# Kernel optimization log

Hardware: AMD Instinct MI355X
Metric: run time of the kernel (lower is better)

Reference implementation:

```python
import jax, jax.numpy as jnp
import numpy as np

N_NODES = 100000
N_EDGES = 3200000
IN_F = 128


def gcn_conv(x, edge_index, edge_weight, W, b):
    """PyG GCNConv: add self-loops (weight 1), symmetric normalization,
    scatter-add aggregation from src -> dst, then bias."""
    n = x.shape[0]
    src, dst = edge_index[0], edge_index[1]
    h = x @ W  # [N, out]
    # degree with self-loop weight 1
    deg = jax.ops.segment_sum(edge_weight, dst, num_segments=n) + 1.0
    dinv = jax.lax.rsqrt(deg)
    norm = dinv[src] * edge_weight * dinv[dst]  # [E]
    msgs = norm[:, None] * h[src]  # [E, out]
    out = jax.ops.segment_sum(msgs, dst, num_segments=n)
    # self-loop contribution: norm = dinv*1*dinv = 1/deg
    out = out + h / deg[:, None]
    return out + b


def setup_inputs() -> dict:
    key = jax.random.key(0)
    ks = jax.random.split(key, 12)
    x = jax.random.normal(ks[0], (N_NODES, IN_F), dtype=jnp.float32)
    edge_index = jax.random.randint(ks[1], (2, N_EDGES), 0, N_NODES)
    edge_weights = jax.random.uniform(ks[2], (N_EDGES,), dtype=jnp.float32)
    def glorot(k, shape):
        lim = np.sqrt(6.0 / (shape[0] + shape[1]))
        return jax.random.uniform(k, shape, jnp.float32, -lim, lim)
    return {
        "x": x,
        "edge_index": edge_index,
        "edge_weights": edge_weights,
        "W1": glorot(ks[3], (IN_F, 32)),
        "b1": jnp.zeros((32,), jnp.float32),
        "W2": glorot(ks[4], (32, 16)),
        "b2": jnp.zeros((16,), jnp.float32),
        "fc1_w": glorot(ks[5], (16, 1)),
        "fc1_b": jnp.zeros((1,), jnp.float32),
        "fc2_w": glorot(ks[6], (33, 1)),
        "fc2_b": jnp.zeros((1,), jnp.float32),
    }


def reference(x, edge_index, edge_weights, W1, b1, W2, b2, fc1_w, fc1_b, fc2_w, fc2_b):
    x1 = gcn_conv(x, edge_index, edge_weights, W1, b1)
    h = jax.nn.relu(x1)  # dropout is identity in eval mode
    x2 = gcn_conv(h, edge_index, edge_weights, W2, b2)
    x1f = x2 @ fc1_w + fc1_b        # [N, 1]
    c = jax.nn.sigmoid(x1f)
    cat = jnp.concatenate([h, c], axis=1)  # [N, 33]
    r = cat @ fc2_w + fc2_b         # [N, 1]
    return (r, x1f)
```

## Files before the change

kernel.cpp:

```cpp
#include <hip/hip_runtime.h>
#include <math.h>


#define TPB 256
#define PA_CHUNK 4096
#define KMAXB 512
#define NPW 8

__global__ __launch_bounds__(512) void countA_kernel(const int* __restrict__ dst,
                                                     int* __restrict__ gtot,
                                                     int E, int K) {
    __shared__ int lhist[KMAXB];
    const int tid = threadIdx.x;
    const int e0  = blockIdx.x * PA_CHUNK;
    if (tid < KMAXB) lhist[tid] = 0;
    __syncthreads();
#pragma unroll
    for (int i = 0; i < 8; ++i) {
        int e = e0 + tid + i * 512;
        if (e < E) atomicAdd(&lhist[dst[e] >> 8], 1);
    }
    __syncthreads();
    if (tid < K && lhist[tid] > 0) atomicAdd(&gtot[tid], lhist[tid]);
}

__global__ __launch_bounds__(64) void kscan_kernel(const int* __restrict__ gtot,
                                                   int* __restrict__ gstart,
                                                   int* __restrict__ gcursor,
                                                   int K, int E) {
    int tid = threadIdx.x;
    int b0 = tid * 8, v[8], s = 0;
#pragma unroll
    for (int t = 0; t < 8; ++t) {
        v[t] = s;
        int idx = b0 + t;
        s += (idx < K) ? gtot[idx] : 0;
    }
    int incl = s;
#pragma unroll
    for (int d = 1; d < 64; d <<= 1) {
        int t2 = __shfl_up(incl, d);
        if (tid >= d) incl += t2;
    }
    int excl = incl - s;
#pragma unroll
    for (int t = 0; t < 8; ++t) {
        int idx = b0 + t;
        if (idx < K) { gstart[idx] = excl + v[t]; gcursor[idx] = excl + v[t]; }
    }
    if (tid == 63) gstart[K] = E;
}

__global__ __launch_bounds__(512) void placeA_kernel(const int* __restrict__ src,
                                                     const int* __restrict__ dst,
                                                     const float* __restrict__ ew,
                                                     uint2* __restrict__ tmp,
                                                     int* __restrict__ gcursor,
                                                     int E, int K) {
    __shared__ int lhist[KMAXB], lbase[KMAXB], lcur[KMAXB], gbaseS[KMAXB];
    __shared__ int ltot;
    __shared__ uint2 stage[PA_CHUNK];
    __shared__ int   saddr[PA_CHUNK];
    const int tid = threadIdx.x;
    const int e0  = blockIdx.x * PA_CHUNK;

    if (tid < KMAXB) { lhist[tid] = 0; lcur[tid] = 0; }
    __syncthreads();

    int   b[8];
    uint2 p[8];
#pragma unroll
    for (int i = 0; i < 8; ++i) {
        int e = e0 + tid + i * 512;
        b[i] = -1;
        if (e < E) {
            int d   = dst[e];
            int s   = src[e];
            float w = ew[e];
            b[i]   = d >> 8;
            p[i].x = __float_as_uint(w);
            p[i].y = ((unsigned)s << 8) | (unsigned)(d & 255);
            atomicAdd(&lhist[b[i]], 1);
        }
    }
    __syncthreads();

    if (tid < 64) {
        int b0 = tid * 8, v[8], s = 0;
#pragma unroll
        for (int t = 0; t < 8; ++t) { v[t] = s; s += lhist[b0 + t]; }
        int incl = s;
#pragma unroll
        for (int d = 1; d < 64; d <<= 1) {
            int t2 = __shfl_up(incl, d);
            if (tid >= d) incl += t2;
        }
        int excl = incl - s;
#pragma unroll
        for (int t = 0; t < 8; ++t) lbase[b0 + t] = excl + v[t];
        if (tid == 63) ltot = incl;
    }
    __syncthreads();

    if (tid < K && lhist[tid] > 0)
        gbaseS[tid] = atomicAdd(&gcursor[tid], lhist[tid]);
    __syncthreads();

#pragma unroll
    for (int i = 0; i < 8; ++i) {
        if (b[i] >= 0) {
            int r    = atomicAdd(&lcur[b[i]], 1);
            int sidx = lbase[b[i]] + r;
            stage[sidx] = p[i];
            saddr[sidx] = gbaseS[b[i]] + r;
        }
    }
    __syncthreads();

    int tot = ltot;
    for (int s = tid; s < tot; s += 512) tmp[saddr[s]] = stage[s];
}

__global__ __launch_bounds__(512) void partB_kernel(const uint2* __restrict__ tmp,
                                                    const int* __restrict__ gstart,
                                                    int2* __restrict__ epair,
                                                    int* __restrict__ off,
                                                    float* __restrict__ dinv,
                                                    int N) {
    __shared__ int   lhist[256], loff[256], lcur[256];
    __shared__ float ldeg[256];
    const int tid  = threadIdx.x;
    const int k    = blockIdx.x;
    const int seg0 = gstart[k], seg1 = gstart[k + 1];

    if (tid < 256) { lhist[tid] = 0; lcur[tid] = 0; ldeg[tid] = 0.f; }
    __syncthreads();

    for (int j = seg0 + tid; j < seg1; j += 512)
        atomicAdd(&lhist[tmp[j].y & 255u], 1);
    __syncthreads();

    if (tid < 64) {
        int b0 = tid * 4, v[4], s = 0;
#pragma unroll
        for (int t = 0; t < 4; ++t) { v[t] = s; s += lhist[b0 + t]; }
        int incl = s;
#pragma unroll
        for (int d = 1; d < 64; d <<= 1) {
            int t2 = __shfl_up(incl, d);
            if (tid >= d) incl += t2;
        }
        int excl = incl - s;
#pragma unroll
        for (int t = 0; t < 4; ++t) loff[b0 + t] = excl + v[t];
    }
    __syncthreads();

    if (tid < 256) {
        int d = (k << 8) + tid;
        if (d < N) off[d] = seg0 + loff[tid];
    }

    for (int j = seg0 + tid; j < seg1; j += 512) {
        uint2 q  = tmp[j];
        int dlow = q.y & 255u;
        int s    = (int)(q.y >> 8);
        float w  = __uint_as_float(q.x);
        int r    = atomicAdd(&lcur[dlow], 1);
        int2 pr; pr.x = s; pr.y = (int)q.x;
        epair[seg0 + loff[dlow] + r] = pr;
        atomicAdd(&ldeg[dlow], w);
    }
    __syncthreads();

    if (tid < 256) {
        int d = (k << 8) + tid;
        if (d < N) dinv[d] = 1.0f / sqrtf(ldeg[tid] + 1.0f);
    }
}

__global__ __launch_bounds__(TPB) void gemm1_kernel(const float* __restrict__ x,
                                                    const float* __restrict__ W,
                                                    const float* __restrict__ dinv,
                                                    float* __restrict__ h, int N) {
    __shared__ float Ws[128 * 32];
    __shared__ float xs[32 * 129];
    const int tid = threadIdx.x;
    const int nb  = blockIdx.x * 32;

    const float4* W4  = (const float4*)W;
    float4*       Ws4 = (float4*)Ws;
#pragma unroll
    for (int i = 0; i < 4; ++i) Ws4[tid + i * 256] = W4[tid + i * 256];

#pragma unroll
    for (int i = 0; i < 4; ++i) {
        int idx  = tid + i * 256;
        int node = idx >> 5;
        int col4 = idx & 31;
        if (nb + node < N) {
            float4 v = ((const float4*)(x + (size_t)nb * 128))[idx];
            float* p = &xs[node * 129 + col4 * 4];
            p[0] = v.x; p[1] = v.y; p[2] = v.z; p[3] = v.w;
        }
    }
    __syncthreads();

    const int nl = tid >> 3;
    const int og = (tid & 7) * 4;
    float a0 = 0.f, a1 = 0.f, a2 = 0.f, a3 = 0.f;
#pragma unroll 8
    for (int k = 0; k < 128; ++k) {
        float xv = xs[nl * 129 + k];
        const float* wp = &Ws[k * 32 + og];
        a0 = fmaf(xv, wp[0], a0);
        a1 = fmaf(xv, wp[1], a1);
        a2 = fmaf(xv, wp[2], a2);
        a3 = fmaf(xv, wp[3], a3);
    }
    int node = nb + nl;
    if (node < N) {
        float dv = dinv[node];
        float* out = &h[(size_t)node * 32 + og];
        out[0] = a0 * dv; out[1] = a1 * dv; out[2] = a2 * dv; out[3] = a3 * dv;
    }
}

__global__ __launch_bounds__(TPB) void gather32_fused_kernel(
    const int* __restrict__ off, const int2* __restrict__ epair,
    const float* __restrict__ g1, const float* __restrict__ dinv,
    const float* __restrict__ b1, const float* __restrict__ W2,
    const float* __restrict__ fc1_w, const float* __restrict__ fc2_w,
    float* __restrict__ z, float* __restrict__ rdot, int N, int E) {
    __shared__ float wls[560];
    const int tid = threadIdx.x;
    wls[tid]       = W2[tid];
    wls[tid + 256] = W2[tid + 256];
    if (tid < 32)      wls[512 + tid] = fc2_w[tid];
    else if (tid < 48) wls[512 + tid] = fc1_w[tid - 32];
    __syncthreads();

    const int lane = tid & 63;
    const int f    = lane & 31;
    const int half = lane >> 5;
    const float bv = b1[f];
    const int wbase = (lane < 16) ? lane : 512;
    const int wstrd = (lane < 16) ? 16 : 1;
    const float f1v = wls[544 + (lane & 15)];

    const int i0 = (blockIdx.x * (TPB / 64) + (tid >> 6)) * NPW;

    for (int t = 0; t < NPW; ++t) {
        int i = i0 + t;
        if (i >= N) return;
        const int s0 = off[i];
        const int s1 = (i + 1 < N) ? off[i + 1] : E;

        float acc = 0.f;
        int j = s0 + half;
        for (; j + 6 < s1; j += 8) {
            int2 pa = epair[j];
            int2 pb = epair[j + 2];
            int2 pc = epair[j + 4];
            int2 pd = epair[j + 6];
            acc = fmaf(__int_as_float(pa.y), g1[(size_t)pa.x * 32 + f], acc);
            acc = fmaf(__int_as_float(pb.y), g1[(size_t)pb.x * 32 + f], acc);
            acc = fmaf(__int_as_float(pc.y), g1[(size_t)pc.x * 32 + f], acc);
            acc = fmaf(__int_as_float(pd.y), g1[(size_t)pd.x * 32 + f], acc);
        }
        for (; j < s1; j += 2) {
            int2 p = epair[j];
            acc = fmaf(__int_as_float(p.y), g1[(size_t)p.x * 32 + f], acc);
        }
        acc += __shfl_xor(acc, 32);

        float dv = dinv[i];
        float v  = fmaxf(dv * (acc + g1[(size_t)i * 32 + f]) + bv, 0.f);

        float hs = 0.f;
#pragma unroll
        for (int k = 0; k < 32; ++k)
            hs = fmaf(__shfl(v, k), wls[wbase + k * wstrd], hs);

        float zp = hs * dv * f1v;
        zp += __shfl_xor(zp, 1);
        zp += __shfl_xor(zp, 2);
        zp += __shfl_xor(zp, 4);
        zp += __shfl_xor(zp, 8);

        if (lane == 0)       z[i]    = zp;
        else if (lane == 16) rdot[i] = hs;
    }
}

__global__ __launch_bounds__(TPB) void final_scalar_kernel(
    const int* __restrict__ off, const int2* __restrict__ epair,
    const float* __restrict__ z, const float* __restrict__ rdot,
    const float* __restrict__ dinv, const float* __restrict__ b2,
    const float* __restrict__ fc1_w, const float* __restrict__ fc1_b,
    const float* __restrict__ fc2_w, const float* __restrict__ fc2_b,
    float* __restrict__ out, int N, int E) {
    const int tid  = threadIdx.x;
    const int lane = tid & 63;

    float C = fc1_b[0];
#pragma unroll
    for (int f = 0; f < 16; ++f) C = fmaf(b2[f], fc1_w[f], C);
    const float f2w = fc2_w[32];
    const float f2b = fc2_b[0];

    const int i0 = (blockIdx.x * (TPB / 64) + (tid >> 6)) * NPW;

    for (int t = 0; t < NPW; ++t) {
        int i = i0 + t;
        if (i >= N) return;
        const int s0 = off[i];
        const int s1 = (i + 1 < N) ? off[i + 1] : E;

        float acc = 0.f;
        for (int j = s0 + lane; j < s1; j += 64) {
            int2 p = epair[j];
            acc = fmaf(__int_as_float(p.y), z[p.x], acc);
        }
        acc += __shfl_xor(acc, 1);
        acc += __shfl_xor(acc, 2);
        acc += __shfl_xor(acc, 4);
        acc += __shfl_xor(acc, 8);
        acc += __shfl_xor(acc, 16);
        acc += __shfl_xor(acc, 32);

        float x1f = dinv[i] * (acc + z[i]) + C;
        float c   = 1.0f / (1.0f + expf(-x1f));
        float r   = fmaf(c, f2w, f2b) + rdot[i];

        if (lane == 0) {
            out[i]     = r;
            out[N + i] = x1f;
        }
    }
}

extern "C" void kernel_launch(void* const* d_in, const int* in_sizes, int n_in,
                              void* d_out, int out_size, void* d_ws, size_t ws_size,
                              hipStream_t stream) {
    const float* x     = (const float*)d_in[0];
    const int*   ei    = (const int*)d_in[1];
    const float* ew    = (const float*)d_in[2];
    const float* W1    = (const float*)d_in[3];
    const float* b1    = (const float*)d_in[4];
    const float* W2    = (const float*)d_in[5];
    const float* b2    = (const float*)d_in[6];
    const float* fc1_w = (const float*)d_in[7];
    const float* fc1_b = (const float*)d_in[8];
    const float* fc2_w = (const float*)d_in[9];
    const float* fc2_b = (const float*)d_in[10];

    const int N = in_sizes[0] / 128;
    const int E = in_sizes[2];
    const int* src = ei;
    const int* dst = ei + E;
    const int K = (N + 255) >> 8;

    float* ws    = (float*)d_ws;
    float* dinv  = ws;
    float* big   = dinv + N;
    float* g1    = big;
    float* rdot  = big + (size_t)48 * N;
    float* z     = big + (size_t)49 * N;
    int*   off   = (int*)(big + (size_t)64 * N);
    int2*  epair = (int2*)(off + N);
    int*   gcursor = (int*)(epair + E);
    int*   gstart  = gcursor + K;
    uint2* tmp   = (uint2*)big;

    size_t need = ((size_t)66 * N + (size_t)2 * E + 2 * K + 2) * 4;
    if (ws_size < need || K > KMAXB || (size_t)E > (size_t)32 * N) return;

    hipMemsetAsync(gcursor, 0, (size_t)K * sizeof(int), stream);

    countA_kernel<<<(E + PA_CHUNK - 1) / PA_CHUNK, 512, 0, stream>>>(dst, gcursor, E, K);
    kscan_kernel<<<1, 64, 0, stream>>>(gcursor, gstart, gcursor, K, E);
    placeA_kernel<<<(E + PA_CHUNK - 1) / PA_CHUNK, 512, 0, stream>>>(
        src, dst, ew, tmp, gcursor, E, K);
    partB_kernel<<<K, 512, 0, stream>>>(tmp, gstart, epair, off, dinv, N);

    gemm1_kernel<<<(N + 31) / 32, TPB, 0, stream>>>(x, W1, dinv, g1, N);

    const int gblocks = (N + 4 * NPW - 1) / (4 * NPW);
    gather32_fused_kernel<<<gblocks, TPB, 0, stream>>>(
        off, epair, g1, dinv, b1, W2, fc1_w, fc2_w, z, rdot, N, E);
    final_scalar_kernel<<<gblocks, TPB, 0, stream>>>(
        off, epair, z, rdot, dinv, b2, fc1_w, fc1_b, fc2_w, fc2_b,
        (float*)d_out, N, E);
}
```

Measured before the change: 350.3 us.

## Fuse edge placement with first GEMM and sort buckets in-place via LDS

Shrinks destination buckets from 256 to 128 nodes so each bucket's edges fit in LDS during the second partition pass. That pass now sorts in place in the edge buffer instead of writing a separate pair array, and spills to scratch when a bucket overflows. The unscaled first-layer GEMM runs as extra blocks of the placement kernel, so the two overlap. The dinv scaling of g1 moves into the partition kernel as a read-modify-write. In exchange, the partition kernel does extra global traffic on g1, and the fused kernel uses larger shared memory, which may lower occupancy.

After: 359.6 us. 1.03x slower.

```diff
diff --git a/kernel.cpp b/kernel.cpp
--- a/kernel.cpp
+++ b/kernel.cpp
@@ -3,8 +3,12 @@
 
 
 #define TPB 256
-#define PA_CHUNK 4096
-#define KMAXB 512
+#define CNT_CHUNK 4096
+#define PLC_CHUNK 3584
+#define KMAXB 1024
+#define BSH 7
+#define BMSK 127
+#define PB_CAP 6912
 #define NPW 8
 
 __global__ __launch_bounds__(512) void countA_kernel(const int* __restrict__ dst,
@@ -12,26 +16,28 @@
                                                      int E, int K) {
     __shared__ int lhist[KMAXB];
     const int tid = threadIdx.x;
-    const int e0  = blockIdx.x * PA_CHUNK;
-    if (tid < KMAXB) lhist[tid] = 0;
+    const int e0  = blockIdx.x * CNT_CHUNK;
+    lhist[tid] = 0; lhist[tid + 512] = 0;
     __syncthreads();
 #pragma unroll
     for (int i = 0; i < 8; ++i) {
         int e = e0 + tid + i * 512;
-        if (e < E) atomicAdd(&lhist[dst[e] >> 8], 1);
+        if (e < E) atomicAdd(&lhist[dst[e] >> BSH], 1);
     }
     __syncthreads();
-    if (tid < K && lhist[tid] > 0) atomicAdd(&gtot[tid], lhist[tid]);
+    for (int b = tid; b < K; b += 512)
+        if (lhist[b] > 0) atomicAdd(&gtot[b], lhist[b]);
 }
 
 __global__ __launch_bounds__(64) void kscan_kernel(const int* __restrict__ gtot,
                                                    int* __restrict__ gstart,
                                                    int* __restrict__ gcursor,
+                                                   int* __restrict__ spill,
                                                    int K, int E) {
     int tid = threadIdx.x;
-    int b0 = tid * 8, v[8], s = 0;
-#pragma unroll
-    for (int t = 0; t < 8; ++t) {
+    int b0 = tid * 13, v[13], s = 0;
+#pragma unroll
+    for (int t = 0; t < 13; ++t) {
         v[t] = s;
         int idx = b0 + t;
         s += (idx < K) ? gtot[idx] : 0;
@@ -44,185 +50,237 @@
     }
     int excl = incl - s;
 #pragma unroll
-    for (int t = 0; t < 8; ++t) {
+    for (int t = 0; t < 13; ++t) {
         int idx = b0 + t;
         if (idx < K) { gstart[idx] = excl + v[t]; gcursor[idx] = excl + v[t]; }
     }
-    if (tid == 63) gstart[K] = E;
-}
-
-__global__ __launch_bounds__(512) void placeA_kernel(const int* __restrict__ src,
+    if (tid == 0) { gstart[K] = E; spill[0] = 0; }
+}
+
+__global__ __launch_bounds__(512) void fusedA_kernel(const int* __restrict__ src,
                                                      const int* __restrict__ dst,
                                                      const float* __restrict__ ew,
-                                                     uint2* __restrict__ tmp,
+                                                     uint2* __restrict__ ebuf,
                                                      int* __restrict__ gcursor,
-                                                     int E, int K) {
-    __shared__ int lhist[KMAXB], lbase[KMAXB], lcur[KMAXB], gbaseS[KMAXB];
-    __shared__ int ltot;
-    __shared__ uint2 stage[PA_CHUNK];
-    __shared__ int   saddr[PA_CHUNK];
+                                                     const float* __restrict__ x,
+                                                     const float* __restrict__ W,
+                                                     float* __restrict__ h,
+                                                     int E, int K, int N, int PB) {
+    __shared__ __align__(16) char smem[59392];
     const int tid = threadIdx.x;
-    const int e0  = blockIdx.x * PA_CHUNK;
-
-    if (tid < KMAXB) { lhist[tid] = 0; lcur[tid] = 0; }
-    __syncthreads();
-
-    int   b[8];
-    uint2 p[8];
-#pragma unroll
-    for (int i = 0; i < 8; ++i) {
-        int e = e0 + tid + i * 512;
-        b[i] = -1;
-        if (e < E) {
-            int d   = dst[e];
-            int s   = src[e];
-            float w = ew[e];
-            b[i]   = d >> 8;
-            p[i].x = __float_as_uint(w);
-            p[i].y = ((unsigned)s << 8) | (unsigned)(d & 255);
-            atomicAdd(&lhist[b[i]], 1);
-        }
-    }
-    __syncthreads();
-
-    if (tid < 64) {
-        int b0 = tid * 8, v[8], s = 0;
-#pragma unroll
-        for (int t = 0; t < 8; ++t) { v[t] = s; s += lhist[b0 + t]; }
-        int incl = s;
-#pragma unroll
-        for (int d = 1; d < 64; d <<= 1) {
-            int t2 = __shfl_up(incl, d);
-            if (tid >= d) incl += t2;
-        }
-        int excl = incl - s;
-#pragma unroll
-        for (int t = 0; t < 8; ++t) lbase[b0 + t] = excl + v[t];
-        if (tid == 63) ltot = incl;
-    }
-    __syncthreads();
-
-    if (tid < K && lhist[tid] > 0)
-        gbaseS[tid] = atomicAdd(&gcursor[tid], lhist[tid]);
-    __syncthreads();
-
-#pragma unroll
-    for (int i = 0; i < 8; ++i) {
-        if (b[i] >= 0) {
-            int r    = atomicAdd(&lcur[b[i]], 1);
-            int sidx = lbase[b[i]] + r;
-            stage[sidx] = p[i];
-            saddr[sidx] = gbaseS[b[i]] + r;
-        }
-    }
-    __syncthreads();
-
-    int tot = ltot;
-    for (int s = tid; s < tot; s += 512) tmp[saddr[s]] = stage[s];
-}
-
-__global__ __launch_bounds__(512) void partB_kernel(const uint2* __restrict__ tmp,
+
+    if ((int)blockIdx.x < PB) {
+        int*   lhist  = (int*)smem;
+        int*   lbase  = (int*)(smem + 4096);
+        int*   lcur   = (int*)(smem + 8192);
+        int*   gbaseS = (int*)(smem + 12288);
+        uint2* stage  = (uint2*)(smem + 16384);
+        int*   saddr  = (int*)(smem + 45056);
+        const int e0 = blockIdx.x * PLC_CHUNK;
+
+        lhist[tid] = 0; lhist[tid + 512] = 0;
+        lcur[tid]  = 0; lcur[tid + 512]  = 0;
+        __syncthreads();
+
+        int   b[7];
+        uint2 p[7];
+#pragma unroll
+        for (int i = 0; i < 7; ++i) {
+            int e = e0 + tid + i * 512;
+            b[i] = -1;
+            if (e < E) {
+                int d   = dst[e];
+                b[i]   = d >> BSH;
+                p[i].x = __float_as_uint(ew[e]);
+                p[i].y = ((unsigned)src[e] << BSH) | (unsigned)(d & BMSK);
+                atomicAdd(&lhist[b[i]], 1);
+            }
+        }
+        __syncthreads();
+
+        __shared__ int ltot;
+        if (tid < 64) {
+            int b0 = tid * 16, v[16], s = 0;
+#pragma unroll
+            for (int t = 0; t < 16; ++t) { v[t] = s; s += lhist[b0 + t]; }
+            int incl = s;
+#pragma unroll
+            for (int d = 1; d < 64; d <<= 1) {
+                int t2 = __shfl_up(incl, d);
+                if (tid >= d) incl += t2;
+            }
+            int excl = incl - s;
+#pragma unroll
+            for (int t = 0; t < 16; ++t) lbase[b0 + t] = excl + v[t];
+            if (tid == 63) ltot = incl;
+        }
+        __syncthreads();
+
+        for (int bk = tid; bk < K; bk += 512)
+            if (lhist[bk] > 0) gbaseS[bk] = atomicAdd(&gcursor[bk], lhist[bk]);
+        __syncthreads();
+
+#pragma unroll
+        for (int i = 0; i < 7; ++i) {
+            if (b[i] >= 0) {
+                int r    = atomicAdd(&lcur[b[i]], 1);
+                int sidx = lbase[b[i]] + r;
+                stage[sidx] = p[i];
+                saddr[sidx] = gbaseS[b[i]] + r;
+            }
+        }
+        __syncthreads();
+
+        int tot = ltot;
+        for (int s = tid; s < tot; s += 512) ebuf[saddr[s]] = stage[s];
+    } else {
+        float* Ws = (float*)smem;
+        float* xs = (float*)smem + 4096;
+        const int nb = ((int)blockIdx.x - PB) * 64;
+
+        const float4* W4  = (const float4*)W;
+        float4*       Ws4 = (float4*)Ws;
+#pragma unroll
+        for (int i = 0; i < 2; ++i) Ws4[tid + i * 512] = W4[tid + i * 512];
+
+#pragma unroll
+        for (int i = 0; i < 4; ++i) {
+            int idx  = tid + i * 512;
+            int node = idx >> 5;
+            int col4 = idx & 31;
+            if (nb + node < N) {
+                float4 v = ((const float4*)(x + (size_t)nb * 128))[idx];
+                float* p = &xs[node * 129 + col4 * 4];
+                p[0] = v.x; p[1] = v.y; p[2] = v.z; p[3] = v.w;
+            }
+        }
+        __syncthreads();
+
+        const int nl = tid >> 3;
+        const int og = (tid & 7) * 4;
+        float a0 = 0.f, a1 = 0.f, a2 = 0.f, a3 = 0.f;
+#pragma unroll 8
+        for (int k = 0; k < 128; ++k) {
+            float xv = xs[nl * 129 + k];
+            const float* wp = &Ws[k * 32 + og];
+            a0 = fmaf(xv, wp[0], a0);
+            a1 = fmaf(xv, wp[1], a1);
+            a2 = fmaf(xv, wp[2], a2);
+            a3 = fmaf(xv, wp[3], a3);
+        }
+        int node = nb + nl;
+        if (node < N) {
+            float* out = &h[(size_t)node * 32 + og];
+            out[0] = a0; out[1] = a1; out[2] = a2; out[3] = a3;
+        }
+    }
+}
+
+__global__ __launch_bounds__(512) void partB_kernel(uint2* __restrict__ ebuf,
                                                     const int* __restrict__ gstart,
-                                                    int2* __restrict__ epair,
                                                     int* __restrict__ off,
                                                     float* __restrict__ dinv,
+                                                    float* __restrict__ g1,
+                                                    uint2* __restrict__ scratch,
+                                                    int* __restrict__ spill,
                                                     int N) {
-    __shared__ int   lhist[256], loff[256], lcur[256];
-    __shared__ float ldeg[256];
+    __shared__ uint2 seg[PB_CAP];
+    __shared__ int   lhist[128], loff[128], lcur[128];
+    __shared__ float ldeg[128];
+    __shared__ int   sbase;
     const int tid  = threadIdx.x;
     const int k    = blockIdx.x;
     const int seg0 = gstart[k], seg1 = gstart[k + 1];
-
-    if (tid < 256) { lhist[tid] = 0; lcur[tid] = 0; ldeg[tid] = 0.f; }
+    const int cnt  = seg1 - seg0;
+
+    if (tid < 128) { lhist[tid] = 0; lcur[tid] = 0; ldeg[tid] = 0.f; }
     __syncthreads();
 
-    for (int j = seg0 + tid; j < seg1; j += 512)
-        atomicAdd(&lhist[tmp[j].y & 255u], 1);
+    if (cnt <= PB_CAP) {
+        for (int j = seg0 + tid; j < seg1; j += 512) seg[j - seg0] = ebuf[j];
+        __syncthreads();
+        for (int t = tid; t < cnt; t += 512)
+            atomicAdd(&lhist[seg[t].y & (unsigned)BMSK], 1);
+        __syncthreads();
+
+        if (tid < 64) {
+            int b0 = tid * 2, v0, v1, s;
+            v0 = 0; v1 = lhist[b0]; s = v1 + lhist[b0 + 1];
+            int incl = s;
+#pragma unroll
+            for (int d = 1; d < 64; d <<= 1) {
+                int t2 = __shfl_up(incl, d);
+                if (tid >= d) incl += t2;
+            }
+            int excl = incl - s;
+            loff[b0] = excl + v0; loff[b0 + 1] = excl + v1;
+        }
+        __syncthreads();
+
+        if (tid < 128) {
+            int d = (k << BSH) + tid;
+            if (d < N) off[d] = seg0 + loff[tid];
+        }
+
+        for (int t = tid; t < cnt; t += 512) {
+            uint2 q  = seg[t];
+            int dlow = q.y & (unsigned)BMSK;
+            int r    = atomicAdd(&lcur[dlow], 1);
+            uint2 pr; pr.x = q.y >> BSH; pr.y = q.x;
+            ebuf[seg0 + loff[dlow] + r] = pr;
+            atomicAdd(&ldeg[dlow], __uint_as_float(q.x));
+        }
+        __syncthreads();
+    } else {
+        for (int j = seg0 + tid; j < seg1; j += 512)
+            atomicAdd(&lhist[ebuf[j].y & (unsigned)BMSK], 1);
+        __syncthreads();
+        if (tid < 64) {
+            int b0 = tid * 2, v0, v1, s;
+            v0 = 0; v1 = lhist[b0]; s = v1 + lhist[b0 + 1];
+            int incl = s;
+#pragma unroll
+            for (int d = 1; d < 64; d <<= 1) {
+                int t2 = __shfl_up(incl, d);
+                if (tid >= d) incl += t2;
+            }
+            int excl = incl - s;
+            loff[b0] = excl + v0; loff[b0 + 1] = excl + v1;
+        }
+        __syncthreads();
+        if (tid < 128) {
+            int d = (k << BSH) + tid;
+            if (d < N) off[d] = seg0 + loff[tid];
+        }
+        if (tid == 0) sbase = atomicAdd(spill, cnt);
+        __syncthreads();
+        for (int j = seg0 + tid; j < seg1; j += 512) {
+            uint2 q  = ebuf[j];
+            int dlow = q.y & (unsigned)BMSK;
+            int r    = atomicAdd(&lcur[dlow], 1);
+            scratch[sbase + loff[dlow] + r] = q;
+            atomicAdd(&ldeg[dlow], __uint_as_float(q.x));
+        }
+        __syncthreads();
+        for (int t = tid; t < cnt; t += 512) {
+            uint2 q = scratch[sbase + t];
+            uint2 pr; pr.x = q.y >> BSH; pr.y = q.x;
+            ebuf[seg0 + t] = pr;
+        }
+        __syncthreads();
+    }
+
+    if (tid < 128) ldeg[tid] = 1.0f / sqrtf(ldeg[tid] + 1.0f);
     __syncthreads();
-
-    if (tid < 64) {
-        int b0 = tid * 4, v[4], s = 0;
-#pragma unroll
-        for (int t = 0; t < 4; ++t) { v[t] = s; s += lhist[b0 + t]; }
-        int incl = s;
-#pragma unroll
-        for (int d = 1; d < 64; d <<= 1) {
-            int t2 = __shfl_up(incl, d);
-            if (tid >= d) incl += t2;
-        }
-        int excl = incl - s;
-#pragma unroll
-        for (int t = 0; t < 4; ++t) loff[b0 + t] = excl + v[t];
-    }
-    __syncthreads();
-
-    if (tid < 256) {
-        int d = (k << 8) + tid;
-        if (d < N) off[d] = seg0 + loff[tid];
-    }
-
-    for (int j = seg0 + tid; j < seg1; j += 512) {
-        uint2 q  = tmp[j];
-        int dlow = q.y & 255u;
-        int s    = (int)(q.y >> 8);
-        float w  = __uint_as_float(q.x);
-        int r    = atomicAdd(&lcur[dlow], 1);
-        int2 pr; pr.x = s; pr.y = (int)q.x;
-        epair[seg0 + loff[dlow] + r] = pr;
-        atomicAdd(&ldeg[dlow], w);
-    }
-    __syncthreads();
-
-    if (tid < 256) {
-        int d = (k << 8) + tid;
-        if (d < N) dinv[d] = 1.0f / sqrtf(ldeg[tid] + 1.0f);
-    }
-}
-
-__global__ __launch_bounds__(TPB) void gemm1_kernel(const float* __restrict__ x,
-                                                    const float* __restrict__ W,
-                                                    const float* __restrict__ dinv,
-                                                    float* __restrict__ h, int N) {
-    __shared__ float Ws[128 * 32];
-    __shared__ float xs[32 * 129];
-    const int tid = threadIdx.x;
-    const int nb  = blockIdx.x * 32;
-
-    const float4* W4  = (const float4*)W;
-    float4*       Ws4 = (float4*)Ws;
-#pragma unroll
-    for (int i = 0; i < 4; ++i) Ws4[tid + i * 256] = W4[tid + i * 256];
-
-#pragma unroll
-    for (int i = 0; i < 4; ++i) {
-        int idx  = tid + i * 256;
-        int node = idx >> 5;
-        int col4 = idx & 31;
-        if (nb + node < N) {
-            float4 v = ((const float4*)(x + (size_t)nb * 128))[idx];
-            float* p = &xs[node * 129 + col4 * 4];
-            p[0] = v.x; p[1] = v.y; p[2] = v.z; p[3] = v.w;
-        }
-    }
-    __syncthreads();
-
-    const int nl = tid >> 3;
-    const int og = (tid & 7) * 4;
-    float a0 = 0.f, a1 = 0.f, a2 = 0.f, a3 = 0.f;
-#pragma unroll 8
-    for (int k = 0; k < 128; ++k) {
-        float xv = xs[nl * 129 + k];
-        const float* wp = &Ws[k * 32 + og];
-        a0 = fmaf(xv, wp[0], a0);
-        a1 = fmaf(xv, wp[1], a1);
-        a2 = fmaf(xv, wp[2], a2);
-        a3 = fmaf(xv, wp[3], a3);
-    }
-    int node = nb + nl;
-    if (node < N) {
-        float dv = dinv[node];
-        float* out = &h[(size_t)node * 32 + og];
-        out[0] = a0 * dv; out[1] = a1 * dv; out[2] = a2 * dv; out[3] = a3 * dv;
+    if (tid < 128) {
+        int d = (k << BSH) + tid;
+        if (d < N) dinv[d] = ldeg[tid];
+    }
+    const int base = (k << BSH);
+    for (int t = tid; t < 128 * 32; t += 512) {
+        int nl = t >> 5;
+        int d  = base + nl;
+        if (d < N) g1[(size_t)d * 32 + (t & 31)] *= ldeg[nl];
     }
 }
 
@@ -359,37 +417,41 @@
     const int E = in_sizes[2];
     const int* src = ei;
     const int* dst = ei + E;
-    const int K = (N + 255) >> 8;
+    const int K = (N + BMSK) >> BSH;
 
     float* ws    = (float*)d_ws;
     float* dinv  = ws;
     float* big   = dinv + N;
     float* g1    = big;
+    uint2* scratch = (uint2*)(big + (size_t)32 * N);
     float* rdot  = big + (size_t)48 * N;
     float* z     = big + (size_t)49 * N;
     int*   off   = (int*)(big + (size_t)64 * N);
-    int2*  epair = (int2*)(off + N);
-    int*   gcursor = (int*)(epair + E);
+    uint2* ebuf  = (uint2*)(off + N);
+    int*   gcursor = (int*)(ebuf + E);
     int*   gstart  = gcursor + K;
-    uint2* tmp   = (uint2*)big;
+    int*   spill   = gstart + K + 1;
 
     size_t need = ((size_t)66 * N + (size_t)2 * E + 2 * K + 2) * 4;
-    if (ws_size < need || K > KMAXB || (size_t)E > (size_t)32 * N) return;
+    if (ws_size < need || K > 832 || (size_t)E > (size_t)32 * N) return;
 
     hipMemsetAsync(gcursor, 0, (size_t)K * sizeof(int), stream);
 
-    countA_kernel<<<(E + PA_CHUNK - 1) / PA_CHUNK, 512, 0, stream>>>(dst, gcursor, E, K);
-    kscan_kernel<<<1, 64, 0, stream>>>(gcursor, gstart, gcursor, K, E);
-    placeA_kernel<<<(E + PA_CHUNK - 1) / PA_CHUNK, 512, 0, stream>>>(
-        src, dst, ew, tmp, gcursor, E, K);
-    partB_kernel<<<K, 512, 0, stream>>>(tmp, gstart, epair, off, dinv, N);
-
-    gemm1_kernel<<<(N + 31) / 32, TPB, 0, stream>>>(x, W1, dinv, g1, N);
+    const int CB = (E + CNT_CHUNK - 1) / CNT_CHUNK;
+    const int PB = (E + PLC_CHUNK - 1) / PLC_CHUNK;
+    const int GB = (N + 63) / 64;
+
+    countA_kernel<<<CB, 512, 0, stream>>>(dst, gcursor, E, K);
+    kscan_kernel<<<1, 64, 0, stream>>>(gcursor, gstart, gcursor, spill, K, E);
+    fusedA_kernel<<<PB + GB, 512, 0, stream>>>(src, dst, ew, ebuf, gcursor,
+                                               x, W1, g1, E, K, N, PB);
+    partB_kernel<<<K, 512, 0, stream>>>(ebuf, gstart, off, dinv, g1,
+                                        scratch, spill, N);
 
     const int gblocks = (N + 4 * NPW - 1) / (4 * NPW);
     gather32_fused_kernel<<<gblocks, TPB, 0, stream>>>(
-        off, epair, g1, dinv, b1, W2, fc1_w, fc2_w, z, rdot, N, E);
+        off, (const int2*)ebuf, g1, dinv, b1, W2, fc1_w, fc2_w, z, rdot, N, E);
     final_scalar_kernel<<<gblocks, TPB, 0, stream>>>(
-        off, epair, z, rdot, dinv, b2, fc1_w, fc1_b, fc2_w, fc2_b,
+        off, (const int2*)ebuf, z, rdot, dinv, b2, fc1_w, fc1_b, fc2_w, fc2_b,
         (float*)d_out, N, E);
 }
```
